# Kernel optimization log

Hardware: AMD Instinct MI355X
Metric: run time of the kernel (lower is better)

## Reference

```python
import jax, jax.numpy as jnp
import numpy as np

C = 256
C8 = C // 8
B, H, W = 4, 64, 64


def setup_inputs() -> dict:
    key = jax.random.key(0)
    ks = jax.random.split(key, 8)
    s = 0.02
    return {
        "x": jax.random.normal(ks[0], (B, C, H, W), dtype=jnp.float32),
        "qw": jax.random.normal(ks[1], (C8, C), dtype=jnp.float32) * s,
        "qb": jax.random.normal(ks[2], (C8,), dtype=jnp.float32) * s,
        "kw": jax.random.normal(ks[3], (C8, C), dtype=jnp.float32) * s,
        "kb": jax.random.normal(ks[4], (C8,), dtype=jnp.float32) * s,
        "vw": jax.random.normal(ks[5], (C, C), dtype=jnp.float32) * s,
        "vb": jax.random.normal(ks[6], (C,), dtype=jnp.float32) * s,
        "gamma": jnp.full((1,), 0.1, dtype=jnp.float32),
    }


def reference(x, qw, qb, kw, kb, vw, vb, gamma):
    b, c, h, w = x.shape
    n = h * w
    xf = x.reshape(b, c, n)  # (B, C, N)
    # 1x1 convs == per-pixel linear projections
    q = jnp.einsum('dc,bcn->bnd', qw, xf) + qb  # (B, N, C/8)
    k = jnp.einsum('dc,bcn->bdn', kw, xf) + kb[None, :, None]  # (B, C/8, N)
    v = jnp.einsum('dc,bcn->bdn', vw, xf) + vb[None, :, None]  # (B, C, N)
    scores = jnp.einsum('bnd,bdm->bnm', q, k)  # (B, N, N), no scale (as in source)
    attn = jax.nn.softmax(scores, axis=-1)
    # out[b,c,i] = sum_j v[b,c,j] * attn[b,i,j]
    out = jnp.einsum('bcj,bij->bci', v, attn).reshape(b, c, h, w)
    return x + gamma.reshape(()) * out
```

## Files before the change

### kernel.cpp

```cpp
#include <hip/hip_runtime.h>
#include <hip/hip_bf16.h>
#include <math.h>

#define CC 256
#define NN 4096

typedef __bf16 bf16x8 __attribute__((ext_vector_type(8)));
typedef __bf16 bf16x4 __attribute__((ext_vector_type(4)));
typedef float  f32x4  __attribute__((ext_vector_type(4)));

#define MFMA16x16x32 __builtin_amdgcn_mfma_f32_16x16x32_bf16

__device__ inline float exp2_hw(float x) {
    float r;
    asm("v_exp_f32 %0, %1" : "=v"(r) : "v"(x));
    return r;
}

__global__ __launch_bounds__(256) void xt_kernel(
    const float* __restrict__ x, __bf16* __restrict__ xh, __bf16* __restrict__ xl)
{
    __shared__ float xs[64][65];
    const int t  = threadIdx.x;
    const int n0 = blockIdx.x * 64;
    const int c0 = blockIdx.y * 64;
    const int b  = blockIdx.z;

    const float* xb = x + ((size_t)b * CC + c0) * NN + n0;
    #pragma unroll
    for (int i = 0; i < 4; ++i) {
        const int cc = i * 16 + (t >> 4);
        const int nn = (t & 15) * 4;
        float4 v = *(const float4*)&xb[(size_t)cc * NN + nn];
        xs[cc][nn + 0] = v.x; xs[cc][nn + 1] = v.y;
        xs[cc][nn + 2] = v.z; xs[cc][nn + 3] = v.w;
    }
    __syncthreads();

    const int n  = t >> 2;
    const int cb = (t & 3) * 16;
    bf16x8 h0, h1, l0, l1;
    #pragma unroll
    for (int i = 0; i < 8; ++i) {
        float v = xs[cb + i][n];
        __bf16 hi = (__bf16)v;
        h0[i] = hi; l0[i] = (__bf16)(v - (float)hi);
    }
    #pragma unroll
    for (int i = 0; i < 8; ++i) {
        float v = xs[cb + 8 + i][n];
        __bf16 hi = (__bf16)v;
        h1[i] = hi; l1[i] = (__bf16)(v - (float)hi);
    }
    const size_t o = ((size_t)b * NN + n0 + n) * CC + c0 + cb;
    *(bf16x8*)&xh[o] = h0; *(bf16x8*)&xh[o + 8] = h1;
    *(bf16x8*)&xl[o] = l0; *(bf16x8*)&xl[o + 8] = l1;
}

__global__ void wprep_kernel(
    const float* __restrict__ qw, const float* __restrict__ qb,
    const float* __restrict__ kw, const float* __restrict__ kb,
    const float* __restrict__ vw, const float* __restrict__ vb,
    __bf16* __restrict__ Wh, __bf16* __restrict__ Wl, float* __restrict__ biasF)
{
    const int r = blockIdx.x;
    const int c = threadIdx.x;
    const float L2E = 1.4426950408889634f;
    const float* wsrc; const float* bsrc; int r0; float scale;
    if (r < 32)       { wsrc = qw; bsrc = qb; r0 = r;      scale = L2E; }
    else if (r < 64)  { wsrc = kw; bsrc = kb; r0 = r - 32; scale = 1.f; }
    else              { wsrc = vw; bsrc = vb; r0 = r - 64; scale = 1.f; }
    float v = wsrc[(size_t)r0 * CC + c] * scale;
    __bf16 hi = (__bf16)v;
    Wh[(size_t)r * CC + c] = hi;
    Wl[(size_t)r * CC + c] = (__bf16)(v - (float)hi);
    if (c == 0) biasF[r] = bsrc[r0] * scale;
}

__global__ __launch_bounds__(256) void proj_kernel(
    const __bf16* __restrict__ xh, const __bf16* __restrict__ xl,
    const __bf16* __restrict__ Wh, const __bf16* __restrict__ Wl,
    const float* __restrict__ biasF,
    __bf16* __restrict__ Qb, __bf16* __restrict__ Kb, __bf16* __restrict__ V2)
{
    const int t    = threadIdx.x;
    const int w    = t >> 6;
    const int lane = t & 63;
    const int lrow = lane & 15;
    const int lgrp = lane >> 4;
    const int n0   = blockIdx.x * 64;
    const int rb   = blockIdx.y;
    const int b    = blockIdx.z;
    const int n    = n0 + w * 16 + lrow;

    const __bf16* xhp = xh + ((size_t)b * NN + n) * CC + lgrp * 8;
    const __bf16* xlp = xl + ((size_t)b * NN + n) * CC + lgrp * 8;
    const __bf16* whp = Wh + (size_t)(rb * 80 + lrow) * CC + lgrp * 8;
    const __bf16* wlp = Wl + (size_t)(rb * 80 + lrow) * CC + lgrp * 8;

    f32x4 acc[5];
    #pragma unroll
    for (int rt = 0; rt < 5; ++rt) acc[rt] = f32x4{0.f, 0.f, 0.f, 0.f};

    #pragma unroll
    for (int c0 = 0; c0 < CC; c0 += 32) {
        const bf16x8 bh = *(const bf16x8*)(xhp + c0);
        const bf16x8 bl = *(const bf16x8*)(xlp + c0);
        #pragma unroll
        for (int rt = 0; rt < 5; ++rt) {
            const bf16x8 ah = *(const bf16x8*)(whp + (size_t)rt * 16 * CC + c0);
            const bf16x8 al = *(const bf16x8*)(wlp + (size_t)rt * 16 * CC + c0);
            acc[rt] = MFMA16x16x32(ah, bh, acc[rt], 0, 0, 0);
            acc[rt] = MFMA16x16x32(ah, bl, acc[rt], 0, 0, 0);
            acc[rt] = MFMA16x16x32(al, bh, acc[rt], 0, 0, 0);
        }
    }

    #pragma unroll
    for (int rt = 0; rt < 5; ++rt) {
        const int g0 = rb * 80 + rt * 16 + lgrp * 4;
        const float4 b4 = *(const float4*)&biasF[g0];
        float v0 = acc[rt].x + b4.x, v1 = acc[rt].y + b4.y;
        float v2 = acc[rt].z + b4.z, v3 = acc[rt].w + b4.w;
        if (g0 < 32) {
            bf16x4 o = { (__bf16)v0, (__bf16)v1, (__bf16)v2, (__bf16)v3 };
            *(bf16x4*)&Qb[((size_t)b * NN + n) * 32 + g0] = o;
        } else if (g0 < 64) {
            bf16x4 o = { (__bf16)v0, (__bf16)v1, (__bf16)v2, (__bf16)v3 };
            *(bf16x4*)&Kb[((size_t)b * NN + n) * 32 + (g0 - 32)] = o;
        } else {
            const int c = g0 - 64;
            const size_t base = ((size_t)b * 128 + (n >> 5)) * (CC * 32) + (n & 31);
            V2[base + (size_t)(c + 0) * 32] = (__bf16)v0;
            V2[base + (size_t)(c + 1) * 32] = (__bf16)v1;
            V2[base + (size_t)(c + 2) * 32] = (__bf16)v2;
            V2[base + (size_t)(c + 3) * 32] = (__bf16)v3;
        }
    }
}

__global__ __launch_bounds__(512, 4) void attn_kernel(
    const __bf16* __restrict__ Qb, const __bf16* __restrict__ Kb,
    const __bf16* __restrict__ V2,
    const float* __restrict__ x, const float* __restrict__ gamma,
    float* __restrict__ y)
{
    const int bid  = blockIdx.x;
    const int swz  = (bid & 7) * 64 + (bid >> 3);
    const int b    = swz >> 7;
    const int h    = (swz >> 6) & 1;
    const int qt   = swz & 63;
    const int w    = threadIdx.x >> 6;
    const int lane = threadIdx.x & 63;
    const int lrow = lane & 15;
    const int lgrp = lane >> 4;
    const int qg   = w >> 1;
    const int kh   = w & 1;
    const int c0w  = h * 128 + w * 16;

    __shared__ __align__(16) __bf16 P[2][64][72];
    __shared__ float lsumP[64][2];

    const bf16x8 qf = *(const bf16x8*)&Qb[((size_t)b * NN + qt * 64 + qg * 16 + lrow) * 32 + lgrp * 8];
    const __bf16* Kp = Kb + ((size_t)b * NN + kh * 32 + lrow) * 32 + lgrp * 8;
    const __bf16* Vp = V2 + (size_t)b * 128 * CC * 32 + (size_t)(c0w + lrow) * 32 + lgrp * 8;

    f32x4 O[4];
    #pragma unroll
    for (int g2 = 0; g2 < 4; ++g2) O[g2] = f32x4{0.f, 0.f, 0.f, 0.f};
    float lsum_l = 0.f;
    const f32x4 zf = f32x4{0.f, 0.f, 0.f, 0.f};

    bf16x8 kf0 = *(const bf16x8*)(Kp);
    bf16x8 kf1 = *(const bf16x8*)(Kp + 512);

    for (int jt = 0; jt < 64; ++jt) {
        const bf16x8 vf0 = *(const bf16x8*)(Vp + (2 * jt)     * 8192);
        const bf16x8 vf1 = *(const bf16x8*)(Vp + (2 * jt + 1) * 8192);
        const int kn_off = ((jt + 1) & 63) * 2048;
        const bf16x8 kn0 = *(const bf16x8*)(Kp + kn_off);
        const bf16x8 kn1 = *(const bf16x8*)(Kp + kn_off + 512);

        const f32x4 s0 = MFMA16x16x32(kf0, qf, zf, 0, 0, 0);
        const f32x4 s1 = MFMA16x16x32(kf1, qf, zf, 0, 0, 0);

        float ps = 0.f;
        bf16x4 p0, p1;
        #pragma unroll
        for (int r = 0; r < 4; ++r) {
            float e = exp2_hw(s0[r]); ps += e; p0[r] = (__bf16)e;
        }
        #pragma unroll
        for (int r = 0; r < 4; ++r) {
            float e = exp2_hw(s1[r]); ps += e; p1[r] = (__bf16)e;
        }
        lsum_l += ps;

        const int buf = jt & 1;
        *(bf16x4*)&P[buf][qg * 16 + lrow][kh * 32 + 4 * lgrp]      = p0;
        *(bf16x4*)&P[buf][qg * 16 + lrow][kh * 32 + 16 + 4 * lgrp] = p1;

        asm volatile("s_waitcnt lgkmcnt(0)\n\ts_barrier" ::: "memory");

        #pragma unroll
        for (int g2 = 0; g2 < 4; ++g2) {
            const bf16x8 pb0 = *(const bf16x8*)&P[buf][g2 * 16 + lrow][lgrp * 8];
            const bf16x8 pb1 = *(const bf16x8*)&P[buf][g2 * 16 + lrow][32 + lgrp * 8];
            O[g2] = MFMA16x16x32(vf0, pb0, O[g2], 0, 0, 0);
            O[g2] = MFMA16x16x32(vf1, pb1, O[g2], 0, 0, 0);
        }
        kf0 = kn0; kf1 = kn1;
    }

    lsum_l += __shfl_xor(lsum_l, 16);
    lsum_l += __shfl_xor(lsum_l, 32);
    if (lgrp == 0) lsumP[qg * 16 + lrow][kh] = lsum_l;
    __syncthreads();

    const float gm = gamma[0];
    #pragma unroll
    for (int g2 = 0; g2 < 4; ++g2) {
        const int q = qt * 64 + g2 * 16 + lrow;
        const float rinv = 1.f / (lsumP[g2 * 16 + lrow][0] + lsumP[g2 * 16 + lrow][1]);
        #pragma unroll
        for (int r = 0; r < 4; ++r) {
            const int c = c0w + lgrp * 4 + r;
            const size_t idx = ((size_t)b * CC + c) * NN + q;
            y[idx] = x[idx] + gm * O[g2][r] * rinv;
        }
    }
}

extern "C" void kernel_launch(void* const* d_in, const int* in_sizes, int n_in,
                              void* d_out, int out_size, void* d_ws, size_t ws_size,
                              hipStream_t stream)
{
    const float* x     = (const float*)d_in[0];
    const float* qw    = (const float*)d_in[1];
    const float* qb    = (const float*)d_in[2];
    const float* kw    = (const float*)d_in[3];
    const float* kb    = (const float*)d_in[4];
    const float* vw    = (const float*)d_in[5];
    const float* vb    = (const float*)d_in[6];
    const float* gamma = (const float*)d_in[7];
    float* y = (float*)d_out;

    char* ws = (char*)d_ws;
    __bf16* xh    = (__bf16*)(ws);
    __bf16* xl    = (__bf16*)(ws + 8388608);
    __bf16* Wh    = (__bf16*)(ws + 16777216);
    __bf16* Wl    = (__bf16*)(ws + 16941056);
    float*  biasF = (float*) (ws + 17104896);
    __bf16* Qb    = (__bf16*)(ws + 17825792);
    __bf16* Kb    = (__bf16*)(ws + 18874368);
    __bf16* V2    = (__bf16*)(ws + 19922944);

    hipLaunchKernelGGL(wprep_kernel, dim3(320), dim3(256), 0, stream,
                       qw, qb, kw, kb, vw, vb, Wh, Wl, biasF);
    hipLaunchKernelGGL(xt_kernel, dim3(64, 4, 4), dim3(256), 0, stream, x, xh, xl);
    hipLaunchKernelGGL(proj_kernel, dim3(64, 4, 4), dim3(256), 0, stream,
                       xh, xl, Wh, Wl, biasF, Qb, Kb, V2);
    hipLaunchKernelGGL(attn_kernel, dim3(512), dim3(512), 0, stream,
                       Qb, Kb, V2, x, gamma, y);
}
```

Measured before the change: 196.9 us.

## Fuse transpose into projection, widen attention blocks to all channels, swizzle P

Removes the separate transpose/split kernel and does the bf16 hi/lo split in shared memory inside the projection kernel, which now computes all 320 output rows per 64-pixel tile. The attention kernel now covers all 256 channels per block (two accumulator sets per wave), halving block count and K/score recomputation, with XCD-aware block mapping. The P buffer uses an XOR swizzle with single 16-byte writes, and V columns are permuted to match. Costs are more registers per wave (occupancy lowered to 2) and fewer blocks for 256 CUs.

```diff
diff --git a/kernel.cpp b/kernel.cpp
--- a/kernel.cpp
+++ b/kernel.cpp
@@ -17,44 +17,8 @@
     return r;
 }
 
-__global__ __launch_bounds__(256) void xt_kernel(
-    const float* __restrict__ x, __bf16* __restrict__ xh, __bf16* __restrict__ xl)
-{
-    __shared__ float xs[64][65];
-    const int t  = threadIdx.x;
-    const int n0 = blockIdx.x * 64;
-    const int c0 = blockIdx.y * 64;
-    const int b  = blockIdx.z;
-
-    const float* xb = x + ((size_t)b * CC + c0) * NN + n0;
-    #pragma unroll
-    for (int i = 0; i < 4; ++i) {
-        const int cc = i * 16 + (t >> 4);
-        const int nn = (t & 15) * 4;
-        float4 v = *(const float4*)&xb[(size_t)cc * NN + nn];
-        xs[cc][nn + 0] = v.x; xs[cc][nn + 1] = v.y;
-        xs[cc][nn + 2] = v.z; xs[cc][nn + 3] = v.w;
-    }
-    __syncthreads();
-
-    const int n  = t >> 2;
-    const int cb = (t & 3) * 16;
-    bf16x8 h0, h1, l0, l1;
-    #pragma unroll
-    for (int i = 0; i < 8; ++i) {
-        float v = xs[cb + i][n];
-        __bf16 hi = (__bf16)v;
-        h0[i] = hi; l0[i] = (__bf16)(v - (float)hi);
-    }
-    #pragma unroll
-    for (int i = 0; i < 8; ++i) {
-        float v = xs[cb + 8 + i][n];
-        __bf16 hi = (__bf16)v;
-        h1[i] = hi; l1[i] = (__bf16)(v - (float)hi);
-    }
-    const size_t o = ((size_t)b * NN + n0 + n) * CC + c0 + cb;
-    *(bf16x8*)&xh[o] = h0; *(bf16x8*)&xh[o + 8] = h1;
-    *(bf16x8*)&xl[o] = l0; *(bf16x8*)&xl[o + 8] = l1;
+__device__ inline int kperm(int j) {
+    return ((j & 12) << 1) | ((j & 16) >> 2) | (j & 3);
 }
 
 __global__ void wprep_kernel(
@@ -77,8 +41,8 @@
     if (c == 0) biasF[r] = bsrc[r0] * scale;
 }
 
-__global__ __launch_bounds__(256) void proj_kernel(
-    const __bf16* __restrict__ xh, const __bf16* __restrict__ xl,
+__global__ __launch_bounds__(512) void proj_kernel(
+    const float* __restrict__ x,
     const __bf16* __restrict__ Wh, const __bf16* __restrict__ Wl,
     const float* __restrict__ biasF,
     __bf16* __restrict__ Qb, __bf16* __restrict__ Kb, __bf16* __restrict__ V2)
@@ -89,39 +53,72 @@
     const int lrow = lane & 15;
     const int lgrp = lane >> 4;
     const int n0   = blockIdx.x * 64;
-    const int rb   = blockIdx.y;
-    const int b    = blockIdx.z;
-    const int n    = n0 + w * 16 + lrow;
-
-    const __bf16* xhp = xh + ((size_t)b * NN + n) * CC + lgrp * 8;
-    const __bf16* xlp = xl + ((size_t)b * NN + n) * CC + lgrp * 8;
-    const __bf16* whp = Wh + (size_t)(rb * 80 + lrow) * CC + lgrp * 8;
-    const __bf16* wlp = Wl + (size_t)(rb * 80 + lrow) * CC + lgrp * 8;
-
-    f32x4 acc[5];
-    #pragma unroll
-    for (int rt = 0; rt < 5; ++rt) acc[rt] = f32x4{0.f, 0.f, 0.f, 0.f};
-
-    #pragma unroll
-    for (int c0 = 0; c0 < CC; c0 += 32) {
-        const bf16x8 bh = *(const bf16x8*)(xhp + c0);
-        const bf16x8 bl = *(const bf16x8*)(xlp + c0);
-        #pragma unroll
-        for (int rt = 0; rt < 5; ++rt) {
-            const bf16x8 ah = *(const bf16x8*)(whp + (size_t)rt * 16 * CC + c0);
-            const bf16x8 al = *(const bf16x8*)(wlp + (size_t)rt * 16 * CC + c0);
-            acc[rt] = MFMA16x16x32(ah, bh, acc[rt], 0, 0, 0);
-            acc[rt] = MFMA16x16x32(ah, bl, acc[rt], 0, 0, 0);
-            acc[rt] = MFMA16x16x32(al, bh, acc[rt], 0, 0, 0);
-        }
-    }
-
-    #pragma unroll
-    for (int rt = 0; rt < 5; ++rt) {
-        const int g0 = rb * 80 + rt * 16 + lgrp * 4;
+    const int b    = blockIdx.y;
+    const int nt   = w & 3;
+    const int rp   = w >> 2;
+
+    __shared__ float  xs[64][68];
+    __shared__ __bf16 xbh[64][136];
+    __shared__ __bf16 xbl[64][136];
+
+    f32x4 acc[10];
+    #pragma unroll
+    for (int i = 0; i < 10; ++i) acc[i] = f32x4{0.f, 0.f, 0.f, 0.f};
+
+    for (int ch = 0; ch < 2; ++ch) {
+        for (int cc = 0; cc < 2; ++cc) {
+            __syncthreads();
+            {
+                const float* xg = x + ((size_t)b * CC + ch * 128 + cc * 64) * NN + n0;
+                const int row = t >> 3;
+                const int col = (t & 7) * 8;
+                float4 a0 = *(const float4*)&xg[(size_t)row * NN + col];
+                float4 a1 = *(const float4*)&xg[(size_t)row * NN + col + 4];
+                *(float4*)&xs[row][col]     = a0;
+                *(float4*)&xs[row][col + 4] = a1;
+            }
+            __syncthreads();
+            {
+                const int cn = t & 63;
+                const int cg = t >> 6;
+                bf16x8 h, l;
+                #pragma unroll
+                for (int e = 0; e < 8; ++e) {
+                    float v = xs[cg * 8 + e][cn];
+                    __bf16 hi = (__bf16)v;
+                    h[e] = hi; l[e] = (__bf16)(v - (float)hi);
+                }
+                *(bf16x8*)&xbh[cn][cc * 64 + cg * 8] = h;
+                *(bf16x8*)&xbl[cn][cc * 64 + cg * 8] = l;
+            }
+        }
+        __syncthreads();
+
+        #pragma unroll
+        for (int ks = 0; ks < 4; ++ks) {
+            const bf16x8 bh = *(const bf16x8*)&xbh[nt * 16 + lrow][ks * 32 + lgrp * 8];
+            const bf16x8 bl = *(const bf16x8*)&xbl[nt * 16 + lrow][ks * 32 + lgrp * 8];
+            #pragma unroll
+            for (int i = 0; i < 10; ++i) {
+                const int rt = rp + 2 * i;
+                const size_t ao = (size_t)(rt * 16 + lrow) * CC + ch * 128 + ks * 32 + lgrp * 8;
+                const bf16x8 ah = *(const bf16x8*)&Wh[ao];
+                const bf16x8 al = *(const bf16x8*)&Wl[ao];
+                acc[i] = MFMA16x16x32(ah, bh, acc[i], 0, 0, 0);
+                acc[i] = MFMA16x16x32(ah, bl, acc[i], 0, 0, 0);
+                acc[i] = MFMA16x16x32(al, bh, acc[i], 0, 0, 0);
+            }
+        }
+    }
+
+    const int n = n0 + nt * 16 + lrow;
+    #pragma unroll
+    for (int i = 0; i < 10; ++i) {
+        const int rt = rp + 2 * i;
+        const int g0 = rt * 16 + lgrp * 4;
         const float4 b4 = *(const float4*)&biasF[g0];
-        float v0 = acc[rt].x + b4.x, v1 = acc[rt].y + b4.y;
-        float v2 = acc[rt].z + b4.z, v3 = acc[rt].w + b4.w;
+        const float v0 = acc[i].x + b4.x, v1 = acc[i].y + b4.y;
+        const float v2 = acc[i].z + b4.z, v3 = acc[i].w + b4.w;
         if (g0 < 32) {
             bf16x4 o = { (__bf16)v0, (__bf16)v1, (__bf16)v2, (__bf16)v3 };
             *(bf16x4*)&Qb[((size_t)b * NN + n) * 32 + g0] = o;
@@ -130,7 +127,7 @@
             *(bf16x4*)&Kb[((size_t)b * NN + n) * 32 + (g0 - 32)] = o;
         } else {
             const int c = g0 - 64;
-            const size_t base = ((size_t)b * 128 + (n >> 5)) * (CC * 32) + (n & 31);
+            const size_t base = ((size_t)b * 128 + (n >> 5)) * (CC * 32) + kperm(n & 31);
             V2[base + (size_t)(c + 0) * 32] = (__bf16)v0;
             V2[base + (size_t)(c + 1) * 32] = (__bf16)v1;
             V2[base + (size_t)(c + 2) * 32] = (__bf16)v2;
@@ -139,75 +136,85 @@
     }
 }
 
-__global__ __launch_bounds__(512, 4) void attn_kernel(
+__global__ __launch_bounds__(512, 2) void attn_kernel(
     const __bf16* __restrict__ Qb, const __bf16* __restrict__ Kb,
     const __bf16* __restrict__ V2,
     const float* __restrict__ x, const float* __restrict__ gamma,
     float* __restrict__ y)
 {
     const int bid  = blockIdx.x;
-    const int swz  = (bid & 7) * 64 + (bid >> 3);
-    const int b    = swz >> 7;
-    const int h    = (swz >> 6) & 1;
-    const int qt   = swz & 63;
+    const int xcd  = bid & 7;
+    const int b    = xcd >> 1;
+    const int qt   = (xcd & 1) * 32 + (bid >> 3);
     const int w    = threadIdx.x >> 6;
     const int lane = threadIdx.x & 63;
     const int lrow = lane & 15;
     const int lgrp = lane >> 4;
     const int qg   = w >> 1;
     const int kh   = w & 1;
-    const int c0w  = h * 128 + w * 16;
-
-    __shared__ __align__(16) __bf16 P[2][64][72];
+    const int c0w  = w * 32;
+
+    __shared__ __align__(16) __bf16 P[2][64][64];
     __shared__ float lsumP[64][2];
 
-    const bf16x8 qf = *(const bf16x8*)&Qb[((size_t)b * NN + qt * 64 + qg * 16 + lrow) * 32 + lgrp * 8];
-    const __bf16* Kp = Kb + ((size_t)b * NN + kh * 32 + lrow) * 32 + lgrp * 8;
-    const __bf16* Vp = V2 + (size_t)b * 128 * CC * 32 + (size_t)(c0w + lrow) * 32 + lgrp * 8;
-
-    f32x4 O[4];
-    #pragma unroll
-    for (int g2 = 0; g2 < 4; ++g2) O[g2] = f32x4{0.f, 0.f, 0.f, 0.f};
+    const __bf16* Qbb = Qb + (size_t)b * NN * 32;
+    const __bf16* Kbb = Kb + (size_t)b * NN * 32;
+    const __bf16* Vbb = V2 + (size_t)b * 128 * (CC * 32);
+
+    const bf16x8 qf = *(const bf16x8*)&Qbb[(size_t)(qt * 64 + qg * 16 + lrow) * 32 + lgrp * 8];
+
+    const size_t koff0 = (size_t)(kh * 32 + lrow) * 32 + lgrp * 8;
+    const size_t koff1 = koff0 + 16 * 32;
+    const size_t vbase = (size_t)(c0w + lrow) * 32 + lgrp * 8;
+
+    f32x4 Oa[4], Ob[4];
+    #pragma unroll
+    for (int g2 = 0; g2 < 4; ++g2) { Oa[g2] = f32x4{0.f,0.f,0.f,0.f}; Ob[g2] = f32x4{0.f,0.f,0.f,0.f}; }
     float lsum_l = 0.f;
     const f32x4 zf = f32x4{0.f, 0.f, 0.f, 0.f};
 
-    bf16x8 kf0 = *(const bf16x8*)(Kp);
-    bf16x8 kf1 = *(const bf16x8*)(Kp + 512);
+    const int swz  = 16 * (lrow & 7);
+    char* prow_w   = (char*)&P[0][qg * 16 + lrow][0];
+    const int woff = (kh * 64 + 16 * lgrp) ^ swz;
+
+    bf16x8 kf0 = *(const bf16x8*)&Kbb[koff0];
+    bf16x8 kf1 = *(const bf16x8*)&Kbb[koff1];
 
     for (int jt = 0; jt < 64; ++jt) {
-        const bf16x8 vf0 = *(const bf16x8*)(Vp + (2 * jt)     * 8192);
-        const bf16x8 vf1 = *(const bf16x8*)(Vp + (2 * jt + 1) * 8192);
-        const int kn_off = ((jt + 1) & 63) * 2048;
-        const bf16x8 kn0 = *(const bf16x8*)(Kp + kn_off);
-        const bf16x8 kn1 = *(const bf16x8*)(Kp + kn_off + 512);
+        const size_t vrow = ((size_t)(2 * jt)) * (CC * 32) + vbase;
+        const bf16x8 vf00 = *(const bf16x8*)&Vbb[vrow];
+        const bf16x8 vf01 = *(const bf16x8*)&Vbb[vrow + 16 * 32];
+        const bf16x8 vf10 = *(const bf16x8*)&Vbb[vrow + (size_t)(CC * 32)];
+        const bf16x8 vf11 = *(const bf16x8*)&Vbb[vrow + (size_t)(CC * 32) + 16 * 32];
+        const size_t jn = (size_t)((jt + 1) & 63) * 64 * 32;
+        const bf16x8 kn0 = *(const bf16x8*)&Kbb[jn + koff0];
+        const bf16x8 kn1 = *(const bf16x8*)&Kbb[jn + koff1];
 
         const f32x4 s0 = MFMA16x16x32(kf0, qf, zf, 0, 0, 0);
         const f32x4 s1 = MFMA16x16x32(kf1, qf, zf, 0, 0, 0);
 
         float ps = 0.f;
-        bf16x4 p0, p1;
-        #pragma unroll
-        for (int r = 0; r < 4; ++r) {
-            float e = exp2_hw(s0[r]); ps += e; p0[r] = (__bf16)e;
-        }
-        #pragma unroll
-        for (int r = 0; r < 4; ++r) {
-            float e = exp2_hw(s1[r]); ps += e; p1[r] = (__bf16)e;
-        }
+        bf16x8 pk;
+        #pragma unroll
+        for (int r = 0; r < 4; ++r) { float e = exp2_hw(s0[r]); ps += e; pk[r]     = (__bf16)e; }
+        #pragma unroll
+        for (int r = 0; r < 4; ++r) { float e = exp2_hw(s1[r]); ps += e; pk[4 + r] = (__bf16)e; }
         lsum_l += ps;
 
         const int buf = jt & 1;
-        *(bf16x4*)&P[buf][qg * 16 + lrow][kh * 32 + 4 * lgrp]      = p0;
-        *(bf16x4*)&P[buf][qg * 16 + lrow][kh * 32 + 16 + 4 * lgrp] = p1;
+        *(bf16x8*)(prow_w + buf * 8192 + woff) = pk;
 
         asm volatile("s_waitcnt lgkmcnt(0)\n\ts_barrier" ::: "memory");
 
         #pragma unroll
         for (int g2 = 0; g2 < 4; ++g2) {
-            const bf16x8 pb0 = *(const bf16x8*)&P[buf][g2 * 16 + lrow][lgrp * 8];
-            const bf16x8 pb1 = *(const bf16x8*)&P[buf][g2 * 16 + lrow][32 + lgrp * 8];
-            O[g2] = MFMA16x16x32(vf0, pb0, O[g2], 0, 0, 0);
-            O[g2] = MFMA16x16x32(vf1, pb1, O[g2], 0, 0, 0);
+            const char* prow_r = (const char*)&P[buf][g2 * 16 + lrow][0];
+            const bf16x8 pb0 = *(const bf16x8*)(prow_r + ((16 * lgrp) ^ swz));
+            const bf16x8 pb1 = *(const bf16x8*)(prow_r + ((64 + 16 * lgrp) ^ swz));
+            Oa[g2] = MFMA16x16x32(vf00, pb0, Oa[g2], 0, 0, 0);
+            Oa[g2] = MFMA16x16x32(vf10, pb1, Oa[g2], 0, 0, 0);
+            Ob[g2] = MFMA16x16x32(vf01, pb0, Ob[g2], 0, 0, 0);
+            Ob[g2] = MFMA16x16x32(vf11, pb1, Ob[g2], 0, 0, 0);
         }
         kf0 = kn0; kf1 = kn1;
     }
@@ -224,9 +231,11 @@
         const float rinv = 1.f / (lsumP[g2 * 16 + lrow][0] + lsumP[g2 * 16 + lrow][1]);
         #pragma unroll
         for (int r = 0; r < 4; ++r) {
-            const int c = c0w + lgrp * 4 + r;
-            const size_t idx = ((size_t)b * CC + c) * NN + q;
-            y[idx] = x[idx] + gm * O[g2][r] * rinv;
+            const int c0 = c0w + lgrp * 4 + r;
+            const size_t i0 = ((size_t)b * CC + c0) * NN + q;
+            y[i0] = x[i0] + gm * Oa[g2][r] * rinv;
+            const size_t i1 = ((size_t)b * CC + c0 + 16) * NN + q;
+            y[i1] = x[i1] + gm * Ob[g2][r] * rinv;
         }
     }
 }
@@ -246,20 +255,17 @@
     float* y = (float*)d_out;
 
     char* ws = (char*)d_ws;
-    __bf16* xh    = (__bf16*)(ws);
-    __bf16* xl    = (__bf16*)(ws + 8388608);
-    __bf16* Wh    = (__bf16*)(ws + 16777216);
-    __bf16* Wl    = (__bf16*)(ws + 16941056);
-    float*  biasF = (float*) (ws + 17104896);
-    __bf16* Qb    = (__bf16*)(ws + 17825792);
-    __bf16* Kb    = (__bf16*)(ws + 18874368);
-    __bf16* V2    = (__bf16*)(ws + 19922944);
+    __bf16* Wh    = (__bf16*)(ws);
+    __bf16* Wl    = (__bf16*)(ws + 163840);
+    float*  biasF = (float*) (ws + 327680);
+    __bf16* Qb    = (__bf16*)(ws + 1048576);
+    __bf16* Kb    = (__bf16*)(ws + 2097152);
+    __bf16* V2    = (__bf16*)(ws + 3145728);
 
     hipLaunchKernelGGL(wprep_kernel, dim3(320), dim3(256), 0, stream,
                        qw, qb, kw, kb, vw, vb, Wh, Wl, biasF);
-    hipLaunchKernelGGL(xt_kernel, dim3(64, 4, 4), dim3(256), 0, stream, x, xh, xl);
-    hipLaunchKernelGGL(proj_kernel, dim3(64, 4, 4), dim3(256), 0, stream,
-                       xh, xl, Wh, Wl, biasF, Qb, Kb, V2);
-    hipLaunchKernelGGL(attn_kernel, dim3(512), dim3(512), 0, stream,
+    hipLaunchKernelGGL(proj_kernel, dim3(64, 4), dim3(512), 0, stream,
+                       x, Wh, Wl, biasF, Qb, Kb, V2);
+    hipLaunchKernelGGL(attn_kernel, dim3(256), dim3(512), 0, stream,
                        Qb, Kb, V2, x, gamma, y);
 }
```

New measurement: 178.2 us. 9.5% less time.
